# Kernel optimization log

Hardware: AMD Instinct MI355X
Metric: run time of the kernel (lower is better)

Reference implementation:

```python
import jax, jax.numpy as jnp
import numpy as np

N = 50000       # nodes
E = 800000      # edges (avg degree 16)
D_IN = 128      # input_dim
HID = 128       # hidden_dim
G_FEAT = 32     # g_feat_dim
G = 64          # number of graphs in batch
EPS = 1e-5      # BatchNorm eps


def _lin_init(key, fan_in, fan_out):
    s = 1.0 / np.sqrt(fan_in)
    return jax.random.uniform(key, (fan_in, fan_out), jnp.float32, -s, s)


def setup_inputs() -> dict:
    key = jax.random.key(0)
    ks = jax.random.split(key, 24)
    inp = {
        'x': jax.random.normal(ks[0], (N, D_IN), jnp.float32),
        'edge_index': jax.random.randint(ks[1], (2, E), 0, N, jnp.int64),
        'batch': jnp.sort(jax.random.randint(ks[2], (N,), 0, G, jnp.int64)),
        'g_feats': jax.random.normal(ks[3], (G, G_FEAT), jnp.float32),
    }
    dims = [D_IN, HID, HID]
    k = 4
    for i, din in enumerate(dims):
        inp[f'Wl{i}'] = _lin_init(ks[k], din, HID); k += 1   # lin_l (neighbors, has bias)
        inp[f'bl{i}'] = jnp.zeros((HID,), jnp.float32)
        inp[f'Wr{i}'] = _lin_init(ks[k], din, HID); k += 1   # lin_r (self, no bias in PyG)
        inp[f'gamma{i}'] = jnp.ones((HID,), jnp.float32)
        inp[f'beta{i}'] = jnp.zeros((HID,), jnp.float32)
    inp['W1'] = _lin_init(ks[k], 2 * HID + G_FEAT, HID); k += 1
    inp['b1'] = jnp.zeros((HID,), jnp.float32)
    inp['W2'] = _lin_init(ks[k], HID, HID // 2); k += 1
    inp['b2'] = jnp.zeros((HID // 2,), jnp.float32)
    inp['W3'] = _lin_init(ks[k], HID // 2, 1); k += 1
    inp['b3'] = jnp.zeros((1,), jnp.float32)
    return inp


def _sage_conv(h, src, dst, Wl, bl, Wr):
    # mean-aggregate neighbor messages x_j into target i, then lin_l(agg)+lin_r(self)
    msgs = h[src]  # [E, d] irregular gather
    agg = jax.ops.segment_sum(msgs, dst, num_segments=N)
    cnt = jax.ops.segment_sum(jnp.ones((E,), h.dtype), dst, num_segments=N)
    agg = agg / jnp.clip(cnt, 1.0)[:, None]
    return agg @ Wl + bl + h @ Wr


def _batch_norm(h, gamma, beta):
    mu = jnp.mean(h, axis=0)
    var = jnp.var(h, axis=0)
    return gamma * (h - mu) * jax.lax.rsqrt(var + EPS) + beta


def _forward(x, edge_index, batch, g_feats, convs, head):
    src, dst = edge_index[0], edge_index[1]
    h = x
    for (Wl, bl, Wr, gamma, beta) in convs:
        h = jax.nn.relu(_batch_norm(_sage_conv(h, src, dst, Wl, bl, Wr), gamma, beta))
        # dropout p=0.01: identity in eval/reference mode
    cnt = jnp.clip(jax.ops.segment_sum(jnp.ones((N,), h.dtype), batch, num_segments=G), 1.0)
    hg_mean = jax.ops.segment_sum(h, batch, num_segments=G) / cnt[:, None]
    hg_max = jax.ops.segment_max(h, batch, num_segments=G)
    W1, b1, W2, b2, W3, b3 = head
    m = jnp.concatenate([hg_mean, hg_max, g_feats], axis=1)  # [G, 2*HID+G_FEAT]
    m = jax.nn.relu(m @ W1 + b1)
    m = jax.nn.relu(m @ W2 + b2)
    return (m @ W3 + b3).reshape(-1)  # [G]


def reference(x, edge_index, batch, g_feats,
              Wl0, bl0, Wr0, gamma0, beta0,
              Wl1, bl1, Wr1, gamma1, beta1,
              Wl2, bl2, Wr2, gamma2, beta2,
              W1, b1, W2, b2, W3, b3):
    convs = [(Wl0, bl0, Wr0, gamma0, beta0),
             (Wl1, bl1, Wr1, gamma1, beta1),
             (Wl2, bl2, Wr2, gamma2, beta2)]
    head = (W1, b1, W2, b2, W3, b3)
    return _forward(x, edge_index, batch, g_feats, convs, head)
```

## Files before the change

kernel.cpp:

```cpp
#include <hip/hip_runtime.h>
#include <stdint.h>

#define NN 50000
#define NE 800000
#define HID 128
#define NG 64
#define BN_EPS 1e-5f
#define SCAN_BLOCKS 196
#define GEMM_BLOCKS ((NN + 127) / 128)
#define SC_NB 8
#define SC_BSZ ((NN + SC_NB - 1) / SC_NB)
#define SC_CHUNK 4096
#define SC_CHUNKS ((NE + SC_CHUNK - 1) / SC_CHUNK)

typedef __bf16 bf16x8 __attribute__((ext_vector_type(8)));
typedef float floatx4 __attribute__((ext_vector_type(4)));

__device__ __forceinline__ float b2f(unsigned short u) {
    union { unsigned int i; float f; } x; x.i = ((unsigned int)u) << 16; return x.f;
}
__device__ __forceinline__ float blo(unsigned int d) { return __uint_as_float(d << 16); }
__device__ __forceinline__ float bhi(unsigned int d) { return __uint_as_float(d & 0xffff0000u); }
__device__ __forceinline__ unsigned short f2b(float f) {
    union { float f; unsigned int i; } x; x.f = f; unsigned int i = x.i;
    if ((i & 0x7f800000u) == 0x7f800000u) return (unsigned short)(i >> 16);
    return (unsigned short)((i + 0x7fffu + ((i >> 16) & 1u)) >> 16);
}
__device__ __forceinline__ unsigned int pack2(float f0, float f1) {
    return (((unsigned int)f2b(f1)) << 16) | f2b(f0);
}

__global__ void k_setup(const float* __restrict__ x, unsigned short* xb, int* deg,
                        int* gstart, int* gend, float* bnstats,
                        float* pool_sum, int* pool_max,
                        const float* __restrict__ Wl0, const float* __restrict__ Wr0,
                        const float* __restrict__ Wl1, const float* __restrict__ Wr1,
                        const float* __restrict__ Wl2, const float* __restrict__ Wr2,
                        unsigned short* Bp) {
    int i = blockIdx.x * 256 + threadIdx.x;
    if (i < NN * 64) {
        float2 v = ((const float2*)x)[i];
        ((unsigned int*)xb)[i] = pack2(v.x, v.y);
    }
    if (i < NN) deg[i] = 0;
    if (i < NG) { gstart[i] = NN; gend[i] = -1; }
    if (i < 3 * 256) bnstats[i] = 0.f;
    if (i < NG * HID) { pool_sum[i] = 0.f; pool_max[i] = 0; }
    if (i < 3 * 32768) {
        int layer = i >> 15;
        int r = i & 32767;
        int nt = r >> 12, kk = (r >> 9) & 7, l = (r >> 3) & 63, j = r & 7;
        int k = kk * 32 + (l >> 4) * 8 + j;
        int n = nt * 16 + (l & 15);
        const float* Wl = layer == 0 ? Wl0 : (layer == 1 ? Wl1 : Wl2);
        const float* Wr = layer == 0 ? Wr0 : (layer == 1 ? Wr1 : Wr2);
        Bp[i] = f2b((k < 128) ? Wl[k * 128 + n] : Wr[(k - 128) * 128 + n]);
    }
}

__global__ void k_hist(const int* __restrict__ dst, int* deg) {
    int bucket = blockIdx.x & (SC_NB - 1);
    int chunk = blockIdx.x / SC_NB;
    int lo = bucket * SC_BSZ, hi = lo + SC_BSZ;
    int base = chunk * SC_CHUNK;
#pragma unroll
    for (int i = 0; i < SC_CHUNK / 256; ++i) {
        int e = base + i * 256 + threadIdx.x;
        if (e < NE) {
            int d = dst[e];
            if (d >= lo && d < hi) atomicAdd(&deg[d], 1);
        }
    }
}

__global__ void k_scan1(const int* __restrict__ deg, int* blocksum,
                        const int* __restrict__ batch, int* gstart, int* gend) {
    __shared__ int lds[256];
    int t = threadIdx.x, i = blockIdx.x * 256 + t;
    lds[t] = (i < NN) ? deg[i] : 0;
    if (i < NN) {
        int g = batch[i];
        if (i == 0 || batch[i - 1] != g) atomicMin(&gstart[g], i);
        if (i == NN - 1 || batch[i + 1] != g) atomicMax(&gend[g], i);
    }
    __syncthreads();
    for (int off = 128; off > 0; off >>= 1) {
        if (t < off) lds[t] += lds[t + off];
        __syncthreads();
    }
    if (t == 0) blocksum[blockIdx.x] = lds[0];
}

__global__ void k_scan2(const int* __restrict__ blocksum, int* blockoff, int* row_start) {
    __shared__ int lds[256];
    int t = threadIdx.x;
    int v = (t < SCAN_BLOCKS) ? blocksum[t] : 0;
    lds[t] = v;
    __syncthreads();
    for (int off = 1; off < 256; off <<= 1) {
        int u = (t >= off) ? lds[t - off] : 0;
        __syncthreads();
        lds[t] += u;
        __syncthreads();
    }
    if (t < SCAN_BLOCKS) blockoff[t] = lds[t] - v;
    if (t == 255) row_start[NN] = lds[255];
}

__global__ void k_scan3(const int* __restrict__ deg, const int* __restrict__ blockoff,
                        int* row_start, int* cursor) {
    __shared__ int lds[256];
    int t = threadIdx.x, i = blockIdx.x * 256 + t;
    int v = (i < NN) ? deg[i] : 0;
    lds[t] = v;
    __syncthreads();
    for (int off = 1; off < 256; off <<= 1) {
        int u = (t >= off) ? lds[t - off] : 0;
        __syncthreads();
        lds[t] += u;
        __syncthreads();
    }
    if (i < NN) {
        int ex = blockoff[blockIdx.x] + lds[t] - v;
        row_start[i] = ex;
        cursor[i] = ex;
    }
}

__global__ void k_scatter(const int* __restrict__ src, const int* __restrict__ dst,
                          int* cursor, int* col) {
    int bucket = blockIdx.x & (SC_NB - 1);
    int chunk = blockIdx.x / SC_NB;
    int lo = bucket * SC_BSZ, hi = lo + SC_BSZ;
    int base = chunk * SC_CHUNK;
#pragma unroll
    for (int i = 0; i < SC_CHUNK / 256; ++i) {
        int e = base + i * 256 + threadIdx.x;
        if (e < NE) {
            int d = dst[e];
            if (d >= lo && d < hi) {
                int p = atomicAdd(&cursor[d], 1);
                col[p] = src[e];
            }
        }
    }
}

__global__ void k_fin(const float* __restrict__ bnstat, const float* __restrict__ gamma,
                      const float* __restrict__ beta, float* sc, float* sh) {
    int t = threadIdx.x;
    float mu = bnstat[t] * (1.f / NN);
    float var = bnstat[128 + t] * (1.f / NN) - mu * mu;
    float s = gamma[t] * rsqrtf(var + BN_EPS);
    sc[t] = s;
    sh[t] = beta[t] - mu * s;
}

__global__ void k_agg(const unsigned short* __restrict__ h, const int* __restrict__ row_start,
                      const int* __restrict__ col, const float* __restrict__ sc,
                      const float* __restrict__ sh, unsigned short* __restrict__ agg) {
    int wid = threadIdx.x >> 6, lane = threadIdx.x & 63;
    int slot = lane >> 4, sub = lane & 15;
    int node = (blockIdx.x * 4 + wid) * 4 + slot;
    int s = row_start[node], e = row_start[node + 1];
    bool ap = sc != nullptr;
    float scv[8], shv[8];
    if (ap) {
        const float4* s4 = (const float4*)sc;
        const float4* h4p = (const float4*)sh;
        float4 c0 = s4[sub * 2], c1 = s4[sub * 2 + 1];
        float4 d0 = h4p[sub * 2], d1 = h4p[sub * 2 + 1];
        scv[0] = c0.x; scv[1] = c0.y; scv[2] = c0.z; scv[3] = c0.w;
        scv[4] = c1.x; scv[5] = c1.y; scv[6] = c1.z; scv[7] = c1.w;
        shv[0] = d0.x; shv[1] = d0.y; shv[2] = d0.z; shv[3] = d0.w;
        shv[4] = d1.x; shv[5] = d1.y; shv[6] = d1.z; shv[7] = d1.w;
    }
    auto tf = [&](float f, int i) -> float {
        return ap ? fmaxf(f * scv[i] + shv[i], 0.f) : f;
    };
    const uint4* h4 = (const uint4*)h;
    float a0 = 0.f, a1 = 0.f, a2 = 0.f, a3 = 0.f, a4 = 0.f, a5 = 0.f, a6 = 0.f, a7 = 0.f;
    int j = s;
    for (; j + 2 <= e; j += 2) {
        int u0 = col[j], u1 = col[j + 1];
        uint4 v0 = h4[(size_t)u0 * 16 + sub];
        uint4 v1 = h4[(size_t)u1 * 16 + sub];
        a0 += tf(blo(v0.x), 0) + tf(blo(v1.x), 0);  a1 += tf(bhi(v0.x), 1) + tf(bhi(v1.x), 1);
        a2 += tf(blo(v0.y), 2) + tf(blo(v1.y), 2);  a3 += tf(bhi(v0.y), 3) + tf(bhi(v1.y), 3);
        a4 += tf(blo(v0.z), 4) + tf(blo(v1.z), 4);  a5 += tf(bhi(v0.z), 5) + tf(bhi(v1.z), 5);
        a6 += tf(blo(v0.w), 6) + tf(blo(v1.w), 6);  a7 += tf(bhi(v0.w), 7) + tf(bhi(v1.w), 7);
    }
    if (j < e) {
        int u = col[j];
        uint4 v = h4[(size_t)u * 16 + sub];
        a0 += tf(blo(v.x), 0);  a1 += tf(bhi(v.x), 1);
        a2 += tf(blo(v.y), 2);  a3 += tf(bhi(v.y), 3);
        a4 += tf(blo(v.z), 4);  a5 += tf(bhi(v.z), 5);
        a6 += tf(blo(v.w), 6);  a7 += tf(bhi(v.w), 7);
    }
    float inv = (e > s) ? 1.f / (float)(e - s) : 0.f;
    uint4 o;
    o.x = pack2(a0 * inv, a1 * inv);
    o.y = pack2(a2 * inv, a3 * inv);
    o.z = pack2(a4 * inv, a5 * inv);
    o.w = pack2(a6 * inv, a7 * inv);
    ((uint4*)agg)[(size_t)node * 16 + sub] = o;
}

__device__ __forceinline__ bf16x8 norm8(bf16x8 v, const float* __restrict__ sc,
                                        const float* __restrict__ sh, int cbase) {
    union { bf16x8 v; unsigned short u[8]; } in; in.v = v;
    union { unsigned int u[4]; bf16x8 v; } out;
#pragma unroll
    for (int i = 0; i < 4; ++i) {
        float f0 = fmaxf(b2f(in.u[2 * i]) * sc[cbase + 2 * i] + sh[cbase + 2 * i], 0.f);
        float f1 = fmaxf(b2f(in.u[2 * i + 1]) * sc[cbase + 2 * i + 1] + sh[cbase + 2 * i + 1], 0.f);
        out.u[i] = pack2(f0, f1);
    }
    return out.v;
}

__global__ void __launch_bounds__(256) k_gemm(unsigned short* buf,
                                              const unsigned short* h,
                                              const unsigned short* __restrict__ Bp,
                                              const float* __restrict__ sc,
                                              const float* __restrict__ sh,
                                              float* bnstat) {
    __shared__ unsigned short Bs[32768];
    int t = threadIdx.x;
    {
        const uint4* s4 = (const uint4*)Bp;
        uint4* d4 = (uint4*)Bs;
        for (int i = t; i < 4096; i += 256) d4[i] = s4[i];
    }
    __syncthreads();
    int wid = t >> 6, lane = t & 63;
    int m = lane & 15, q = lane >> 4;
    int mbase = blockIdx.x * 128 + wid * 32;
    bool active = mbase < NN;
    bool ap = sc != nullptr;
    float s8[8] = {0, 0, 0, 0, 0, 0, 0, 0};
    float ss8[8] = {0, 0, 0, 0, 0, 0, 0, 0};
    if (active) {
        int row0 = mbase + m;
        int row1 = min(mbase + 16 + m, NN - 1);
        const bf16x8* Abuf = (const bf16x8*)buf;
        const bf16x8* Ah = (const bf16x8*)h;
        size_t b0 = (size_t)row0 * 16, b1 = (size_t)row1 * 16;
        bf16x8 af0[8], af1[8];
#pragma unroll
        for (int kk = 0; kk < 4; ++kk) {
            af0[kk] = Abuf[b0 + kk * 4 + q];
            af1[kk] = Abuf[b1 + kk * 4 + q];
            bf16x8 h0 = Ah[b0 + kk * 4 + q];
            bf16x8 h1 = Ah[b1 + kk * 4 + q];
            if (ap) {
                int cb = kk * 32 + q * 8;
                h0 = norm8(h0, sc, sh, cb);
                h1 = norm8(h1, sc, sh, cb);
            }
            af0[4 + kk] = h0;
            af1[4 + kk] = h1;
        }
        const bf16x8* B = (const bf16x8*)Bs;
        floatx4 acc[2][8];
#pragma unroll
        for (int mt = 0; mt < 2; ++mt)
#pragma unroll
            for (int nt = 0; nt < 8; ++nt) acc[mt][nt] = (floatx4){0.f, 0.f, 0.f, 0.f};
#pragma unroll
        for (int kk = 0; kk < 8; ++kk) {
#pragma unroll
            for (int nt = 0; nt < 8; ++nt) {
                bf16x8 b = B[(nt * 8 + kk) * 64 + lane];
                acc[0][nt] = __builtin_amdgcn_mfma_f32_16x16x32_bf16(af0[kk], b, acc[0][nt], 0, 0, 0);
                acc[1][nt] = __builtin_amdgcn_mfma_f32_16x16x32_bf16(af1[kk], b, acc[1][nt], 0, 0, 0);
            }
        }
#pragma unroll
        for (int mt = 0; mt < 2; ++mt)
#pragma unroll
            for (int nt = 0; nt < 8; ++nt) {
                int c = nt * 16 + m;
#pragma unroll
                for (int reg = 0; reg < 4; ++reg) {
                    int r = mbase + mt * 16 + q * 4 + reg;
                    if (r < NN) {
                        float v = acc[mt][nt][reg];
                        buf[(size_t)r * 128 + c] = f2b(v);
                        s8[nt] += v;
                        ss8[nt] += v * v;
                    }
                }
            }
#pragma unroll
        for (int nt = 0; nt < 8; ++nt) {
            s8[nt] += __shfl_xor(s8[nt], 16, 64);  s8[nt] += __shfl_xor(s8[nt], 32, 64);
            ss8[nt] += __shfl_xor(ss8[nt], 16, 64); ss8[nt] += __shfl_xor(ss8[nt], 32, 64);
        }
    }
    __syncthreads();
    float* stf = (float*)Bs;
    if (t < 256) stf[t] = 0.f;
    __syncthreads();
    if (active && lane < 16) {
#pragma unroll
        for (int nt = 0; nt < 8; ++nt) {
            int c = nt * 16 + m;
            atomicAdd(&stf[c], s8[nt]);
            atomicAdd(&stf[128 + c], ss8[nt]);
        }
    }
    __syncthreads();
    if (t < 256) atomicAdd(&bnstat[t], stf[t]);
}

__global__ void k_pool(const unsigned short* __restrict__ h, const int* __restrict__ gstart,
                       const int* __restrict__ gend, const float* __restrict__ sc,
                       const float* __restrict__ sh, float* pool_sum, int* pool_max) {
    int g = blockIdx.x >> 3, chunk = blockIdx.x & 7;
    int s = gstart[g], e = gend[g];
    if (s > e) return;
    int cnt = e - s + 1;
    int per = (cnt + 7) >> 3;
    int r0 = s + chunk * per;
    int r1 = min(r0 + per, e + 1);
    int c = threadIdx.x & 127, half = threadIdx.x >> 7;
    float scc = sc[c], shc = sh[c];
    float sm = 0.f, mx = 0.f;
    for (int r = r0 + half; r < r1; r += 2) {
        float v = fmaxf(b2f(h[(size_t)r * 128 + c]) * scc + shc, 0.f);
        sm += v;
        mx = fmaxf(mx, v);
    }
    atomicAdd(&pool_sum[g * 128 + c], sm);
    atomicMax(&pool_max[g * 128 + c], __float_as_int(mx));
}

__global__ void __launch_bounds__(128) k_head(
    const float* __restrict__ pool_sum, const int* __restrict__ pool_max,
    const int* __restrict__ gstart, const int* __restrict__ gend,
    const float* __restrict__ gfeats,
    const float* __restrict__ W1, const float* __restrict__ bs1,
    const float* __restrict__ W2, const float* __restrict__ bs2,
    const float* __restrict__ W3, const float* __restrict__ bs3,
    float* out) {
    __shared__ float m[288];
    __shared__ float o1[128];
    __shared__ float o2[64];
    int g = blockIdx.x, t = threadIdx.x;
    int s = gstart[g], e = gend[g];
    int cint = e - s + 1;
    float cnt = (float)(cint < 1 ? 1 : cint);
    if (t < 128) {
        m[t] = pool_sum[g * 128 + t] / cnt;
        m[128 + t] = __int_as_float(pool_max[g * 128 + t]);
    }
    if (t < 32) m[256 + t] = gfeats[g * 32 + t];
    __syncthreads();
    float acc = bs1[t];
    for (int k = 0; k < 288; ++k) acc += m[k] * W1[k * 128 + t];
    o1[t] = fmaxf(acc, 0.f);
    __syncthreads();
    if (t < 64) {
        float a2 = bs2[t];
        for (int k = 0; k < 128; ++k) a2 += o1[k] * W2[k * 64 + t];
        o2[t] = fmaxf(a2, 0.f);
    }
    __syncthreads();
    if (t < 64) {
        float p = o2[t] * W3[t];
#pragma unroll
        for (int off = 32; off; off >>= 1) p += __shfl_down(p, off, 64);
        if (t == 0) out[g] = p + bs3[0];
    }
}

extern "C" void kernel_launch(void* const* d_in, const int* in_sizes, int n_in,
                              void* d_out, int out_size, void* d_ws, size_t ws_size,
                              hipStream_t stream) {
    const float* x = (const float*)d_in[0];
    const int* ei = (const int*)d_in[1];
    const int* batch = (const int*)d_in[2];
    const float* gfeats = (const float*)d_in[3];
    const float *Wl[3], *Wr[3], *gma[3], *bta[3];
    for (int i = 0; i < 3; ++i) {
        Wl[i] = (const float*)d_in[4 + 5 * i];
        Wr[i] = (const float*)d_in[6 + 5 * i];
        gma[i] = (const float*)d_in[7 + 5 * i];
        bta[i] = (const float*)d_in[8 + 5 * i];
    }
    const float* W1 = (const float*)d_in[19];
    const float* bs1 = (const float*)d_in[20];
    const float* W2 = (const float*)d_in[21];
    const float* bs2 = (const float*)d_in[22];
    const float* W3 = (const float*)d_in[23];
    const float* bs3 = (const float*)d_in[24];

    char* p = (char*)d_ws;
    auto alloc = [&](size_t bytes) -> char* {
        char* r = p;
        p += (bytes + 255) & ~(size_t)255;
        return r;
    };
    int* deg = (int*)alloc(NN * 4);
    int* row_start = (int*)alloc((NN + 1) * 4);
    int* cursor = (int*)alloc(NN * 4);
    int* col = (int*)alloc(NE * 4);
    int* gstart = (int*)alloc(NG * 4);
    int* gend = (int*)alloc(NG * 4);
    float* bnstats = (float*)alloc(3 * 256 * 4);
    float* scbuf = (float*)alloc(3 * 128 * 4);
    float* shbuf = (float*)alloc(3 * 128 * 4);
    float* pool_sum = (float*)alloc(NG * HID * 4);
    int* pool_max = (int*)alloc(NG * HID * 4);
    int* blocksum = (int*)alloc(SCAN_BLOCKS * 4);
    int* blockoff = (int*)alloc(SCAN_BLOCKS * 4);
    unsigned short* Bp = (unsigned short*)alloc(3 * 32768 * 2);
    unsigned short* xb = (unsigned short*)alloc((size_t)NN * 128 * 2);
    unsigned short* b0 = (unsigned short*)alloc((size_t)NN * 128 * 2);
    unsigned short* b1 = (unsigned short*)alloc((size_t)NN * 128 * 2);

    const int* srcv = ei;
    const int* dstv = ei + NE;

    k_setup<<<(NN * 64 + 255) / 256, 256, 0, stream>>>(
        x, xb, deg, gstart, gend, bnstats, pool_sum, pool_max,
        Wl[0], Wr[0], Wl[1], Wr[1], Wl[2], Wr[2], Bp);
    k_hist<<<SC_CHUNKS * SC_NB, 256, 0, stream>>>(dstv, deg);
    k_scan1<<<SCAN_BLOCKS, 256, 0, stream>>>(deg, blocksum, batch, gstart, gend);
    k_scan2<<<1, 256, 0, stream>>>(blocksum, blockoff, row_start);
    k_scan3<<<SCAN_BLOCKS, 256, 0, stream>>>(deg, blockoff, row_start, cursor);
    k_scatter<<<SC_CHUNKS * SC_NB, 256, 0, stream>>>(srcv, dstv, cursor, col);

    const unsigned short* hin = xb;
    unsigned short* work[3] = {b0, b1, b0};
    for (int l = 0; l < 3; ++l) {
        unsigned short* w = work[l];
        const float* scp = (l == 0) ? nullptr : scbuf + (l - 1) * 128;
        const float* shp = (l == 0) ? nullptr : shbuf + (l - 1) * 128;
        k_agg<<<(NN + 15) / 16, 256, 0, stream>>>(hin, row_start, col, scp, shp, w);
        k_gemm<<<GEMM_BLOCKS, 256, 0, stream>>>(w, hin, Bp + l * 32768, scp, shp,
                                                bnstats + l * 256);
        k_fin<<<1, 128, 0, stream>>>(bnstats + l * 256, gma[l], bta[l],
                                     scbuf + l * 128, shbuf + l * 128);
        hin = w;
    }
    k_pool<<<NG * 8, 256, 0, stream>>>(hin, gstart, gend, scbuf + 2 * 128, shbuf + 2 * 128,
                                       pool_sum, pool_max);
    k_head<<<NG, 128, 0, stream>>>(pool_sum, pool_max, gstart, gend, gfeats,
                                   W1, bs1, W2, bs2, W3, bs3, (float*)d_out);
}
```

Before: 414.0 us.

## Partition neighbor gathers into source-range passes and fuse BN finalize into consumers

```diff
diff --git a/kernel.cpp b/kernel.cpp
--- a/kernel.cpp
+++ b/kernel.cpp
@@ -12,6 +12,7 @@
 #define SC_BSZ ((NN + SC_NB - 1) / SC_NB)
 #define SC_CHUNK 4096
 #define SC_CHUNKS ((NE + SC_CHUNK - 1) / SC_CHUNK)
+#define AGG_PASSES 4
 
 typedef __bf16 bf16x8 __attribute__((ext_vector_type(8)));
 typedef float floatx4 __attribute__((ext_vector_type(4)));
@@ -28,6 +29,14 @@
 }
 __device__ __forceinline__ unsigned int pack2(float f0, float f1) {
     return (((unsigned int)f2b(f1)) << 16) | f2b(f0);
+}
+__device__ __forceinline__ float2 bn_pair(const float* __restrict__ bnstat,
+                                          const float* __restrict__ gamma,
+                                          const float* __restrict__ beta, int c) {
+    float mu = bnstat[c] * (1.f / NN);
+    float var = bnstat[128 + c] * (1.f / NN) - mu * mu;
+    float s = gamma[c] * rsqrtf(var + BN_EPS);
+    return make_float2(s, beta[c] - mu * s);
 }
 
 __global__ void k_setup(const float* __restrict__ x, unsigned short* xb, int* deg,
@@ -146,57 +155,63 @@
     }
 }
 
-__global__ void k_fin(const float* __restrict__ bnstat, const float* __restrict__ gamma,
-                      const float* __restrict__ beta, float* sc, float* sh) {
-    int t = threadIdx.x;
-    float mu = bnstat[t] * (1.f / NN);
-    float var = bnstat[128 + t] * (1.f / NN) - mu * mu;
-    float s = gamma[t] * rsqrtf(var + BN_EPS);
-    sc[t] = s;
-    sh[t] = beta[t] - mu * s;
-}
-
 __global__ void k_agg(const unsigned short* __restrict__ h, const int* __restrict__ row_start,
-                      const int* __restrict__ col, const float* __restrict__ sc,
-                      const float* __restrict__ sh, unsigned short* __restrict__ agg) {
+                      const int* __restrict__ col, const float* __restrict__ bnstat,
+                      const float* __restrict__ gamma, const float* __restrict__ beta,
+                      unsigned short* __restrict__ agg) {
     int wid = threadIdx.x >> 6, lane = threadIdx.x & 63;
     int slot = lane >> 4, sub = lane & 15;
     int node = (blockIdx.x * 4 + wid) * 4 + slot;
     int s = row_start[node], e = row_start[node + 1];
-    bool ap = sc != nullptr;
+    bool ap = bnstat != nullptr;
     float scv[8], shv[8];
     if (ap) {
-        const float4* s4 = (const float4*)sc;
-        const float4* h4p = (const float4*)sh;
-        float4 c0 = s4[sub * 2], c1 = s4[sub * 2 + 1];
-        float4 d0 = h4p[sub * 2], d1 = h4p[sub * 2 + 1];
-        scv[0] = c0.x; scv[1] = c0.y; scv[2] = c0.z; scv[3] = c0.w;
-        scv[4] = c1.x; scv[5] = c1.y; scv[6] = c1.z; scv[7] = c1.w;
-        shv[0] = d0.x; shv[1] = d0.y; shv[2] = d0.z; shv[3] = d0.w;
-        shv[4] = d1.x; shv[5] = d1.y; shv[6] = d1.z; shv[7] = d1.w;
+#pragma unroll
+        for (int i = 0; i < 8; ++i) {
+            float2 p = bn_pair(bnstat, gamma, beta, sub * 8 + i);
+            scv[i] = p.x; shv[i] = p.y;
+        }
     }
     auto tf = [&](float f, int i) -> float {
         return ap ? fmaxf(f * scv[i] + shv[i], 0.f) : f;
     };
     const uint4* h4 = (const uint4*)h;
     float a0 = 0.f, a1 = 0.f, a2 = 0.f, a3 = 0.f, a4 = 0.f, a5 = 0.f, a6 = 0.f, a7 = 0.f;
-    int j = s;
-    for (; j + 2 <= e; j += 2) {
-        int u0 = col[j], u1 = col[j + 1];
-        uint4 v0 = h4[(size_t)u0 * 16 + sub];
-        uint4 v1 = h4[(size_t)u1 * 16 + sub];
-        a0 += tf(blo(v0.x), 0) + tf(blo(v1.x), 0);  a1 += tf(bhi(v0.x), 1) + tf(bhi(v1.x), 1);
-        a2 += tf(blo(v0.y), 2) + tf(blo(v1.y), 2);  a3 += tf(bhi(v0.y), 3) + tf(bhi(v1.y), 3);
-        a4 += tf(blo(v0.z), 4) + tf(blo(v1.z), 4);  a5 += tf(bhi(v0.z), 5) + tf(bhi(v1.z), 5);
-        a6 += tf(blo(v0.w), 6) + tf(blo(v1.w), 6);  a7 += tf(bhi(v0.w), 7) + tf(bhi(v1.w), 7);
-    }
-    if (j < e) {
-        int u = col[j];
-        uint4 v = h4[(size_t)u * 16 + sub];
-        a0 += tf(blo(v.x), 0);  a1 += tf(bhi(v.x), 1);
-        a2 += tf(blo(v.y), 2);  a3 += tf(bhi(v.y), 3);
-        a4 += tf(blo(v.z), 4);  a5 += tf(bhi(v.z), 5);
-        a6 += tf(blo(v.w), 6);  a7 += tf(bhi(v.w), 7);
+    const uint4 z = {0u, 0u, 0u, 0u};
+#pragma unroll 1
+    for (int pass = 0; pass < AGG_PASSES; ++pass) {
+        int ulo = (NN / AGG_PASSES) * pass;
+        int uhi = (pass == AGG_PASSES - 1) ? NN : ulo + NN / AGG_PASSES;
+        int j = s;
+        for (; j + 2 <= e; j += 2) {
+            int u0 = col[j], u1 = col[j + 1];
+            bool p0 = (u0 >= ulo) & (u0 < uhi);
+            bool p1 = (u1 >= ulo) & (u1 < uhi);
+            uint4 v0 = p0 ? h4[(size_t)u0 * 16 + sub] : z;
+            uint4 v1 = p1 ? h4[(size_t)u1 * 16 + sub] : z;
+            if (p0) {
+                a0 += tf(blo(v0.x), 0);  a1 += tf(bhi(v0.x), 1);
+                a2 += tf(blo(v0.y), 2);  a3 += tf(bhi(v0.y), 3);
+                a4 += tf(blo(v0.z), 4);  a5 += tf(bhi(v0.z), 5);
+                a6 += tf(blo(v0.w), 6);  a7 += tf(bhi(v0.w), 7);
+            }
+            if (p1) {
+                a0 += tf(blo(v1.x), 0);  a1 += tf(bhi(v1.x), 1);
+                a2 += tf(blo(v1.y), 2);  a3 += tf(bhi(v1.y), 3);
+                a4 += tf(blo(v1.z), 4);  a5 += tf(bhi(v1.z), 5);
+                a6 += tf(blo(v1.w), 6);  a7 += tf(bhi(v1.w), 7);
+            }
+        }
+        if (j < e) {
+            int u = col[j];
+            if (u >= ulo && u < uhi) {
+                uint4 v = h4[(size_t)u * 16 + sub];
+                a0 += tf(blo(v.x), 0);  a1 += tf(bhi(v.x), 1);
+                a2 += tf(blo(v.y), 2);  a3 += tf(bhi(v.y), 3);
+                a4 += tf(blo(v.z), 4);  a5 += tf(bhi(v.z), 5);
+                a6 += tf(blo(v.w), 6);  a7 += tf(bhi(v.w), 7);
+            }
+        }
     }
     float inv = (e > s) ? 1.f / (float)(e - s) : 0.f;
     uint4 o;
@@ -207,8 +222,7 @@
     ((uint4*)agg)[(size_t)node * 16 + sub] = o;
 }
 
-__device__ __forceinline__ bf16x8 norm8(bf16x8 v, const float* __restrict__ sc,
-                                        const float* __restrict__ sh, int cbase) {
+__device__ __forceinline__ bf16x8 norm8(bf16x8 v, const float* sc, const float* sh, int cbase) {
     union { bf16x8 v; unsigned short u[8]; } in; in.v = v;
     union { unsigned int u[4]; bf16x8 v; } out;
 #pragma unroll
@@ -223,22 +237,28 @@
 __global__ void __launch_bounds__(256) k_gemm(unsigned short* buf,
                                               const unsigned short* h,
                                               const unsigned short* __restrict__ Bp,
-                                              const float* __restrict__ sc,
-                                              const float* __restrict__ sh,
+                                              const float* __restrict__ pbnstat,
+                                              const float* __restrict__ pgamma,
+                                              const float* __restrict__ pbeta,
                                               float* bnstat) {
     __shared__ unsigned short Bs[32768];
+    __shared__ float s_sc[128], s_sh[128];
     int t = threadIdx.x;
     {
         const uint4* s4 = (const uint4*)Bp;
         uint4* d4 = (uint4*)Bs;
         for (int i = t; i < 4096; i += 256) d4[i] = s4[i];
     }
+    bool ap = pbnstat != nullptr;
+    if (ap && t < 128) {
+        float2 p = bn_pair(pbnstat, pgamma, pbeta, t);
+        s_sc[t] = p.x; s_sh[t] = p.y;
+    }
     __syncthreads();
     int wid = t >> 6, lane = t & 63;
     int m = lane & 15, q = lane >> 4;
     int mbase = blockIdx.x * 128 + wid * 32;
     bool active = mbase < NN;
-    bool ap = sc != nullptr;
     float s8[8] = {0, 0, 0, 0, 0, 0, 0, 0};
     float ss8[8] = {0, 0, 0, 0, 0, 0, 0, 0};
     if (active) {
@@ -256,8 +276,8 @@
             bf16x8 h1 = Ah[b1 + kk * 4 + q];
             if (ap) {
                 int cb = kk * 32 + q * 8;
-                h0 = norm8(h0, sc, sh, cb);
-                h1 = norm8(h1, sc, sh, cb);
+                h0 = norm8(h0, s_sc, s_sh, cb);
+                h1 = norm8(h1, s_sc, s_sh, cb);
             }
             af0[4 + kk] = h0;
             af1[4 + kk] = h1;
@@ -316,8 +336,9 @@
 }
 
 __global__ void k_pool(const unsigned short* __restrict__ h, const int* __restrict__ gstart,
-                       const int* __restrict__ gend, const float* __restrict__ sc,
-                       const float* __restrict__ sh, float* pool_sum, int* pool_max) {
+                       const int* __restrict__ gend, const float* __restrict__ bnstat,
+                       const float* __restrict__ gamma, const float* __restrict__ beta,
+                       float* pool_sum, int* pool_max) {
     int g = blockIdx.x >> 3, chunk = blockIdx.x & 7;
     int s = gstart[g], e = gend[g];
     if (s > e) return;
@@ -326,10 +347,10 @@
     int r0 = s + chunk * per;
     int r1 = min(r0 + per, e + 1);
     int c = threadIdx.x & 127, half = threadIdx.x >> 7;
-    float scc = sc[c], shc = sh[c];
+    float2 pr = bn_pair(bnstat, gamma, beta, c);
     float sm = 0.f, mx = 0.f;
     for (int r = r0 + half; r < r1; r += 2) {
-        float v = fmaxf(b2f(h[(size_t)r * 128 + c]) * scc + shc, 0.f);
+        float v = fmaxf(b2f(h[(size_t)r * 128 + c]) * pr.x + pr.y, 0.f);
         sm += v;
         mx = fmaxf(mx, v);
     }
@@ -410,8 +431,6 @@
     int* gstart = (int*)alloc(NG * 4);
     int* gend = (int*)alloc(NG * 4);
     float* bnstats = (float*)alloc(3 * 256 * 4);
-    float* scbuf = (float*)alloc(3 * 128 * 4);
-    float* shbuf = (float*)alloc(3 * 128 * 4);
     float* pool_sum = (float*)alloc(NG * HID * 4);
     int* pool_max = (int*)alloc(NG * HID * 4);
     int* blocksum = (int*)alloc(SCAN_BLOCKS * 4);
@@ -437,16 +456,15 @@
     unsigned short* work[3] = {b0, b1, b0};
     for (int l = 0; l < 3; ++l) {
         unsigned short* w = work[l];
-        const float* scp = (l == 0) ? nullptr : scbuf + (l - 1) * 128;
-        const float* shp = (l == 0) ? nullptr : shbuf + (l - 1) * 128;
-        k_agg<<<(NN + 15) / 16, 256, 0, stream>>>(hin, row_start, col, scp, shp, w);
-        k_gemm<<<GEMM_BLOCKS, 256, 0, stream>>>(w, hin, Bp + l * 32768, scp, shp,
+        const float* pb = (l == 0) ? nullptr : bnstats + (l - 1) * 256;
+        const float* pg = (l == 0) ? nullptr : gma[l - 1];
+        const float* pt = (l == 0) ? nullptr : bta[l - 1];
+        k_agg<<<(NN + 15) / 16, 256, 0, stream>>>(hin, row_start, col, pb, pg, pt, w);
+        k_gemm<<<GEMM_BLOCKS, 256, 0, stream>>>(w, hin, Bp + l * 32768, pb, pg, pt,
                                                 bnstats + l * 256);
-        k_fin<<<1, 128, 0, stream>>>(bnstats + l * 256, gma[l], bta[l],
-                                     scbuf + l * 128, shbuf + l * 128);
         hin = w;
     }
-    k_pool<<<NG * 8, 256, 0, stream>>>(hin, gstart, gend, scbuf + 2 * 128, shbuf + 2 * 128,
+    k_pool<<<NG * 8, 256, 0, stream>>>(hin, gstart, gend, bnstats + 2 * 256, gma[2], bta[2],
                                        pool_sum, pool_max);
     k_head<<<NG, 128, 0, stream>>>(pool_sum, pool_max, gstart, gend, gfeats,
                                    W1, bs1, W2, bs2, W3, bs3, (float*)d_out);
```

Result: slower. 590.3 us (+42.6%).
